# Kernel optimization log

Hardware: AMD Instinct MI355X
Metric: run time of the kernel (lower is better)

The kernel has to match this reference:

```python
import jax, jax.numpy as jnp
import numpy as np

B, N, D, H, E = 128, 256, 256, 8, 524288
RATIO = 0.5
HD = D // H
K_SEL = int(N * RATIO)  # nodes kept per graph


def setup_inputs() -> dict:
    key = jax.random.key(0)
    ks = jax.random.split(key, 12)
    embeddings = jax.random.normal(ks[0], (B, N, D), dtype=jnp.float32)
    mask = jnp.ones((B, N), dtype=bool)
    dist = jax.random.uniform(ks[1], (B, N, N), dtype=jnp.float32)
    # within-graph random edges, offset per graph
    epg = E // B
    src = jax.random.randint(ks[2], (B, epg), 0, N)
    dst = jax.random.randint(ks[3], (B, epg), 0, N)
    off = (jnp.arange(B) * N)[:, None]
    edge_index = jnp.stack([(src + off).reshape(-1), (dst + off).reshape(-1)]).astype(jnp.int64)
    batch = jnp.repeat(jnp.arange(B, dtype=jnp.int64), N)
    s = 1.0 / np.sqrt(D)
    Wq = jax.random.normal(ks[4], (D, D), jnp.float32) * s
    Wk = jax.random.normal(ks[5], (D, D), jnp.float32) * s
    Wv = jax.random.normal(ks[6], (D, D), jnp.float32) * s
    Wo = jax.random.normal(ks[7], (D, D), jnp.float32) * s
    bq = jnp.zeros((D,), jnp.float32)
    bk = jnp.zeros((D,), jnp.float32)
    bv = jnp.zeros((D,), jnp.float32)
    bo = jnp.zeros((D,), jnp.float32)
    pool_w = jax.random.normal(ks[8], (D,), jnp.float32) * s
    return dict(embeddings=embeddings, mask=mask, dist=dist, edge_index=edge_index,
                batch=batch, Wq=Wq, bq=bq, Wk=Wk, bk=bk, Wv=Wv, bv=bv, Wo=Wo, bo=bo,
                pool_w=pool_w)


def _mha(x, mask, dist, Wq, bq, Wk, bk, Wv, bv, Wo, bo):
    # x: [B,N,D]; dist used as additive attention bias; mask: [B,N] key mask
    q = (x @ Wq + bq).reshape(B, N, H, HD).transpose(0, 2, 1, 3)  # bhnd
    k = (x @ Wk + bk).reshape(B, N, H, HD).transpose(0, 2, 1, 3)
    v = (x @ Wv + bv).reshape(B, N, H, HD).transpose(0, 2, 1, 3)
    scores = jnp.einsum('bhnd,bhmd->bhnm', q, k) / jnp.sqrt(jnp.float32(HD))
    scores = scores + dist[:, None]  # broadcast bias over heads
    scores = jnp.where(mask[:, None, None, :], scores, jnp.float32(-1e9))
    attn = jax.nn.softmax(scores, axis=-1)
    out = jnp.einsum('bhnm,bhmd->bhnd', attn, v)
    out = out.transpose(0, 2, 1, 3).reshape(B, N, D)
    return out @ Wo + bo


def reference(embeddings, mask, dist, edge_index, batch, Wq, bq, Wk, bk, Wv, bv, Wo, bo, pool_w):
    encoder_result = _mha(embeddings, mask, dist, Wq, bq, Wk, bk, Wv, bv, Wo, bo)
    # encoder_result[mask] -> sparse node features; mask is all-true so shape is [B*N, D]
    x = encoder_result.reshape(B * N, D)

    # ---- TopKPooling (PyG semantics): score = x.w/||w||, keep top ceil(ratio*N)/graph ----
    score = (x @ pool_w) / jnp.linalg.norm(pool_w)          # [B*N]
    vals, idx = jax.lax.top_k(score.reshape(B, N), K_SEL)    # per-graph top-k
    perm = (idx + (jnp.arange(B) * N)[:, None]).reshape(-1)  # [B*K] global node ids
    sub_x = x[perm] * jnp.tanh(vals).reshape(-1, 1)
    sub_batch = batch[perm]

    # relabel nodes: new id = position in perm (PyG ordering); dropped -> sentinel
    n_keep = B * K_SEL
    sentinel = n_keep
    new_id = jnp.full((B * N,), sentinel, dtype=edge_index.dtype).at[perm].set(
        jnp.arange(n_keep, dtype=edge_index.dtype))
    row = new_id[edge_index[0]]
    col = new_id[edge_index[1]]
    valid = (row < sentinel) & (col < sentinel)
    row = jnp.where(valid, row, sentinel)
    col = jnp.where(valid, col, sentinel)
    # sort_edge_index: row-major sort; invalid (sentinel) edges pushed to the end
    order = jnp.argsort(row * (sentinel + 1) + col)
    sub_edge_index = jnp.stack([row, col])[:, order]
    return encoder_result, sub_x, sub_edge_index, sub_batch
```

## Files before the change

kernel.cpp:

```cpp
#include <hip/hip_runtime.h>
#include <math.h>

#define Bg   128
#define Ng   256
#define Dg   256
#define Hg   8
#define HDg  32
#define Eg   524288
#define Kg   128
#define BNg  32768
#define SENT 16384

using bf16x8 = __attribute__((ext_vector_type(8))) short;
using f32x4  = __attribute__((ext_vector_type(4))) float;

__device__ inline void split2(float x, short &h, short &l) {
    unsigned u = __float_as_uint(x);
    h = (short)(u >> 16);
    float hf = __uint_as_float(u & 0xffff0000u);
    float r = x - hf;
    l = (short)(__float_as_uint(r) >> 16);
}
__device__ inline unsigned pack2(short a, short b) {
    return (unsigned)(unsigned short)a | ((unsigned)(unsigned short)b << 16);
}
__device__ inline void gload16(const void* g, void* l) {
    __builtin_amdgcn_global_load_lds(
        (const __attribute__((address_space(1))) unsigned*)g,
        (__attribute__((address_space(3))) unsigned*)l, 16, 0, 0);
}

__global__ __launch_bounds__(256) void split_x(
    const float* __restrict__ x, short* __restrict__ xh, short* __restrict__ xl)
{
    size_t i = ((size_t)blockIdx.x * 256 + threadIdx.x) * 8;
    float4 a = *(const float4*)(x + i);
    float4 b = *(const float4*)(x + i + 4);
    float v[8] = {a.x,a.y,a.z,a.w,b.x,b.y,b.z,b.w};
    short h[8], l[8];
    #pragma unroll
    for (int j = 0; j < 8; ++j) split2(v[j], h[j], l[j]);
    uint4 uh, ul;
    uh.x = pack2(h[0],h[1]); uh.y = pack2(h[2],h[3]);
    uh.z = pack2(h[4],h[5]); uh.w = pack2(h[6],h[7]);
    ul.x = pack2(l[0],l[1]); ul.y = pack2(l[2],l[3]);
    ul.z = pack2(l[4],l[5]); ul.w = pack2(l[6],l[7]);
    *(uint4*)(xh + i) = uh;
    *(uint4*)(xl + i) = ul;
}

__global__ __launch_bounds__(256) void wprep(
    const float* __restrict__ Wq, const float* __restrict__ Wk,
    const float* __restrict__ Wv, const float* __restrict__ Wo,
    short* __restrict__ WTh, short* __restrict__ WTl)
{
    __shared__ float t[64][65];
    const int bid = blockIdx.x;
    const int mat = bid >> 4;
    const int kt = (bid >> 2) & 3, nt = bid & 3;
    const float* W = (mat==0) ? Wq : (mat==1) ? Wk : (mat==2) ? Wv : Wo;
    const int tid = threadIdx.x;
    const int r = tid >> 2, c4 = tid & 3;
    #pragma unroll
    for (int i = 0; i < 4; ++i) {
        float4 v = *(const float4*)(W + (size_t)(kt*64 + r)*256 + nt*64 + c4*16 + i*4);
        t[r][c4*16 + i*4 + 0] = v.x; t[r][c4*16 + i*4 + 1] = v.y;
        t[r][c4*16 + i*4 + 2] = v.z; t[r][c4*16 + i*4 + 3] = v.w;
    }
    __syncthreads();
    const int n = r, k0 = c4 * 16;
    short hb[16], lb[16];
    #pragma unroll
    for (int i = 0; i < 16; ++i) split2(t[k0 + i][n], hb[i], lb[i]);
    size_t base = (size_t)mat*65536 + (size_t)(nt*64 + n)*256 + kt*64 + k0;
    uint4 uh0, uh1, ul0, ul1;
    uh0.x=pack2(hb[0],hb[1]);  uh0.y=pack2(hb[2],hb[3]);  uh0.z=pack2(hb[4],hb[5]);  uh0.w=pack2(hb[6],hb[7]);
    uh1.x=pack2(hb[8],hb[9]);  uh1.y=pack2(hb[10],hb[11]);uh1.z=pack2(hb[12],hb[13]);uh1.w=pack2(hb[14],hb[15]);
    ul0.x=pack2(lb[0],lb[1]);  ul0.y=pack2(lb[2],lb[3]);  ul0.z=pack2(lb[4],lb[5]);  ul0.w=pack2(lb[6],lb[7]);
    ul1.x=pack2(lb[8],lb[9]);  ul1.y=pack2(lb[10],lb[11]);ul1.z=pack2(lb[12],lb[13]);ul1.w=pack2(lb[14],lb[15]);
    *(uint4*)&WTh[base]     = uh0; *(uint4*)&WTh[base + 8] = uh1;
    *(uint4*)&WTl[base]     = ul0; *(uint4*)&WTl[base + 8] = ul1;
}

__global__ __launch_bounds__(512, 4) void qkv_mm(
    const short* __restrict__ xh, const short* __restrict__ xl,
    const short* __restrict__ WTh, const short* __restrict__ WTl,
    const float* __restrict__ bq, const float* __restrict__ bk, const float* __restrict__ bv,
    short* __restrict__ Qh, short* __restrict__ Ql,
    short* __restrict__ Kh, short* __restrict__ Kl,
    short* __restrict__ Vh, short* __restrict__ Vl)
{
    const int z = blockIdx.z;
    const float* bias = (z==0) ? bq : (z==1) ? bk : bv;
    short* outH       = (z==0) ? Qh : (z==1) ? Kh : Vh;
    short* outL       = (z==0) ? Ql : (z==1) ? Kl : Vl;
    const float scale = (z==0) ? 0.17677669529663687f : 1.0f;
    const short* bth = WTh + (size_t)z * 65536;
    const short* btl = WTl + (size_t)z * 65536;
    __shared__ __align__(16) short lds[2][16384];
    const int tid = threadIdx.x;
    const int lane = tid & 63, w = tid >> 6;
    const int g = lane >> 4, li = lane & 15;
    const int wr = w >> 2, wc = w & 3;
    const int m0 = blockIdx.x * 128, n0 = blockIdx.y * 128;
    const int sr = tid >> 2, sc = (tid & 3) * 8;
    const int wbase = w * 512;
    f32x4 acc[4][2];
    #pragma unroll
    for (int i = 0; i < 4; ++i)
        #pragma unroll
        for (int j = 0; j < 2; ++j) acc[i][j] = (f32x4){0.f,0.f,0.f,0.f};

    {
        size_t ga = (size_t)(m0 + sr)*256 + sc;
        size_t gb = (size_t)(n0 + sr)*256 + sc;
        gload16(xh + ga,  &lds[0][        wbase]);
        gload16(xl + ga,  &lds[0][ 4096 + wbase]);
        gload16(bth + gb, &lds[0][ 8192 + wbase]);
        gload16(btl + gb, &lds[0][12288 + wbase]);
    }
    __syncthreads();

    for (int k = 0; k < 8; ++k) {
        const int cur = k & 1;
        if (k < 7) {
            const int nb = cur ^ 1;
            int k0n = (k+1)*32;
            size_t ga = (size_t)(m0 + sr)*256 + k0n + sc;
            size_t gb = (size_t)(n0 + sr)*256 + k0n + sc;
            gload16(xh + ga,  &lds[nb][        wbase]);
            gload16(xl + ga,  &lds[nb][ 4096 + wbase]);
            gload16(bth + gb, &lds[nb][ 8192 + wbase]);
            gload16(btl + gb, &lds[nb][12288 + wbase]);
        }
        bf16x8 ah[4], al[4], bh[2], bl[2];
        #pragma unroll
        for (int i = 0; i < 4; ++i) {
            int row = wr*64 + i*16 + li;
            ah[i] = *(const bf16x8*)&lds[cur][       row*32 + g*8];
            al[i] = *(const bf16x8*)&lds[cur][4096 + row*32 + g*8];
        }
        #pragma unroll
        for (int j = 0; j < 2; ++j) {
            int row = wc*32 + j*16 + li;
            bh[j] = *(const bf16x8*)&lds[cur][ 8192 + row*32 + g*8];
            bl[j] = *(const bf16x8*)&lds[cur][12288 + row*32 + g*8];
        }
        #pragma unroll
        for (int i = 0; i < 4; ++i)
            #pragma unroll
            for (int j = 0; j < 2; ++j) {
                acc[i][j] = __builtin_amdgcn_mfma_f32_16x16x32_bf16(bh[j], ah[i], acc[i][j], 0,0,0);
                acc[i][j] = __builtin_amdgcn_mfma_f32_16x16x32_bf16(bl[j], ah[i], acc[i][j], 0,0,0);
                acc[i][j] = __builtin_amdgcn_mfma_f32_16x16x32_bf16(bh[j], al[i], acc[i][j], 0,0,0);
            }
        __syncthreads();
    }
    #pragma unroll
    for (int i = 0; i < 4; ++i) {
        int mrow = m0 + wr*64 + i*16 + li;
        int b = mrow >> 8, nn = mrow & 255;
        #pragma unroll
        for (int j = 0; j < 2; ++j) {
            int c0 = n0 + wc*32 + j*16 + g*4;
            int h = c0 >> 5, hd = c0 & 31;
            float4 bi = *(const float4*)(bias + c0);
            float v0 = (acc[i][j][0] + bi.x) * scale;
            float v1 = (acc[i][j][1] + bi.y) * scale;
            float v2 = (acc[i][j][2] + bi.z) * scale;
            float v3 = (acc[i][j][3] + bi.w) * scale;
            short h0,l0,h1,l1,h2,l2,h3,l3;
            split2(v0,h0,l0); split2(v1,h1,l1); split2(v2,h2,l2); split2(v3,h3,l3);
            uint2 hiq, loq;
            hiq.x = pack2(h0,h1); hiq.y = pack2(h2,h3);
            loq.x = pack2(l0,l1); loq.y = pack2(l2,l3);
            size_t idx = ((size_t)(b*Hg + h)*Ng + nn)*HDg + hd;
            *(uint2*)&outH[idx] = hiq;
            *(uint2*)&outL[idx] = loq;
        }
    }
}

__global__ __launch_bounds__(512, 4) void attn_mfma(
    const short* __restrict__ Qh, const short* __restrict__ Ql,
    const short* __restrict__ Kh, const short* __restrict__ Kl,
    const short* __restrict__ Vh, const short* __restrict__ Vl,
    const float* __restrict__ dist,
    short* __restrict__ AOh, short* __restrict__ AOl)
{
    __shared__ __align__(16) short Khi [2][32][40];
    __shared__ __align__(16) short Klo [2][32][40];
    __shared__ __align__(16) short Vthi[2][32][40];
    __shared__ __align__(16) short Vtlo[2][32][40];
    __shared__ __align__(16) short Phi [8][32][40];
    __shared__ __align__(16) short Plo [8][32][40];

    const int i0 = blockIdx.x;
    const int xcd = i0 & 7;
    const int m_  = i0 >> 3;
    const int h   = m_ & 7;
    const int b   = (m_ >> 3) * 8 + xcd;
    const int bh  = b * 8 + h;

    const int tid = threadIdx.x;
    const int w = tid >> 6;
    const int lane = tid & 63;
    const int g = lane >> 4;
    const int li = lane & 15;
    const int q0 = w * 32;
    const int skey = tid >> 4;
    const int se0  = (tid & 15) * 2;
    const float* dall = dist + (size_t)b*Ng*Ng;

    bf16x8 qh[2], ql[2];
    #pragma unroll
    for (int tq = 0; tq < 2; ++tq) {
        size_t qoff = ((size_t)bh * Ng + q0 + tq*16 + li) * HDg + g*8;
        qh[tq] = *(const bf16x8*)(Qh + qoff);
        ql[tq] = *(const bf16x8*)(Ql + qoff);
    }

    {
        size_t koff = ((size_t)bh*Ng + skey) * HDg + se0;
        unsigned kh1 = *(const unsigned*)(Kh + koff);
        unsigned kl1 = *(const unsigned*)(Kl + koff);
        unsigned vh1 = *(const unsigned*)(Vh + koff);
        unsigned vl1 = *(const unsigned*)(Vl + koff);
        *(unsigned*)&Khi[0][skey][se0] = kh1;
        *(unsigned*)&Klo[0][skey][se0] = kl1;
        Vthi[0][se0+0][skey] = (short)(vh1 & 0xffff);
        Vthi[0][se0+1][skey] = (short)(vh1 >> 16);
        Vtlo[0][se0+0][skey] = (short)(vl1 & 0xffff);
        Vtlo[0][se0+1][skey] = (short)(vl1 >> 16);
    }
    __syncthreads();

    f32x4 O[2][2];
    #pragma unroll
    for (int tq=0;tq<2;++tq)
        #pragma unroll
        for (int td=0;td<2;++td) O[tq][td] = (f32x4){0.f,0.f,0.f,0.f};
    float lpart[2] = {0.f, 0.f};

    for (int ch = 0; ch < 8; ++ch) {
        const int cur = ch & 1;
        const bool pref = (ch < 7);
        unsigned khr, klr, vhr, vlr;
        if (pref) {
            size_t koff = ((size_t)bh*Ng + (ch+1)*32 + skey) * HDg + se0;
            khr = *(const unsigned*)(Kh + koff);
            klr = *(const unsigned*)(Kl + koff);
            vhr = *(const unsigned*)(Vh + koff);
            vlr = *(const unsigned*)(Vl + koff);
        }
        f32x4 sacc[2][2];
        #pragma unroll
        for (int tq = 0; tq < 2; ++tq)
            #pragma unroll
            for (int tc = 0; tc < 2; ++tc) {
                const float* dp = dall + (size_t)(q0 + tq*16 + li)*Ng + ch*32 + tc*16 + g*4;
                float4 dv = *(const float4*)dp;
                sacc[tq][tc] = (f32x4){dv.x, dv.y, dv.z, dv.w};
            }
        bf16x8 kbh[2], kbl[2];
        #pragma unroll
        for (int tc = 0; tc < 2; ++tc) {
            kbh[tc] = *(const bf16x8*)&Khi[cur][tc*16+li][g*8];
            kbl[tc] = *(const bf16x8*)&Klo[cur][tc*16+li][g*8];
        }
        #pragma unroll
        for (int tq = 0; tq < 2; ++tq)
            #pragma unroll
            for (int tc = 0; tc < 2; ++tc) {
                sacc[tq][tc] = __builtin_amdgcn_mfma_f32_16x16x32_bf16(kbh[tc], qh[tq], sacc[tq][tc], 0,0,0);
                sacc[tq][tc] = __builtin_amdgcn_mfma_f32_16x16x32_bf16(kbl[tc], qh[tq], sacc[tq][tc], 0,0,0);
                sacc[tq][tc] = __builtin_amdgcn_mfma_f32_16x16x32_bf16(kbh[tc], ql[tq], sacc[tq][tc], 0,0,0);
            }
        #pragma unroll
        for (int tq = 0; tq < 2; ++tq)
            #pragma unroll
            for (int tc = 0; tc < 2; ++tc) {
                float p0 = __expf(sacc[tq][tc][0] - 16.f);
                float p1 = __expf(sacc[tq][tc][1] - 16.f);
                float p2 = __expf(sacc[tq][tc][2] - 16.f);
                float p3 = __expf(sacc[tq][tc][3] - 16.f);
                lpart[tq] += p0; lpart[tq] += p1; lpart[tq] += p2; lpart[tq] += p3;
                unsigned u0 = __float_as_uint(p0), u1 = __float_as_uint(p1);
                unsigned u2 = __float_as_uint(p2), u3 = __float_as_uint(p3);
                float r0 = p0 - __uint_as_float(u0 & 0xffff0000u);
                float r1 = p1 - __uint_as_float(u1 & 0xffff0000u);
                float r2 = p2 - __uint_as_float(u2 & 0xffff0000u);
                float r3 = p3 - __uint_as_float(u3 & 0xffff0000u);
                uint2 hiq, loq;
                hiq.x = (u0 >> 16) | (u1 & 0xffff0000u);
                hiq.y = (u2 >> 16) | (u3 & 0xffff0000u);
                loq.x = (__float_as_uint(r0) >> 16) | (__float_as_uint(r1) & 0xffff0000u);
                loq.y = (__float_as_uint(r2) >> 16) | (__float_as_uint(r3) & 0xffff0000u);
                *(uint2*)&Phi[w][tq*16 + li][tc*16 + g*4] = hiq;
                *(uint2*)&Plo[w][tq*16 + li][tc*16 + g*4] = loq;
            }
        bf16x8 vbh[2], vbl[2];
        #pragma unroll
        for (int td = 0; td < 2; ++td) {
            vbh[td] = *(const bf16x8*)&Vthi[cur][td*16+li][g*8];
            vbl[td] = *(const bf16x8*)&Vtlo[cur][td*16+li][g*8];
        }
        #pragma unroll
        for (int tq = 0; tq < 2; ++tq) {
            bf16x8 ph = *(const bf16x8*)&Phi[w][tq*16+li][g*8];
            bf16x8 pl = *(const bf16x8*)&Plo[w][tq*16+li][g*8];
            #pragma unroll
            for (int td = 0; td < 2; ++td) {
                O[tq][td] = __builtin_amdgcn_mfma_f32_16x16x32_bf16(vbh[td], ph, O[tq][td], 0,0,0);
                O[tq][td] = __builtin_amdgcn_mfma_f32_16x16x32_bf16(vbl[td], ph, O[tq][td], 0,0,0);
                O[tq][td] = __builtin_amdgcn_mfma_f32_16x16x32_bf16(vbh[td], pl, O[tq][td], 0,0,0);
            }
        }
        if (pref) {
            const int nb = cur ^ 1;
            *(unsigned*)&Khi[nb][skey][se0] = khr;
            *(unsigned*)&Klo[nb][skey][se0] = klr;
            Vthi[nb][se0+0][skey] = (short)(vhr & 0xffff);
            Vthi[nb][se0+1][skey] = (short)(vhr >> 16);
            Vtlo[nb][se0+0][skey] = (short)(vlr & 0xffff);
            Vtlo[nb][se0+1][skey] = (short)(vlr >> 16);
        }
        __syncthreads();
    }
    float inv[2];
    #pragma unroll
    for (int tq = 0; tq < 2; ++tq) {
        float s = lpart[tq];
        s += __shfl_xor(s, 16);
        s += __shfl_xor(s, 32);
        inv[tq] = 1.f / s;
    }
    #pragma unroll
    for (int tq = 0; tq < 2; ++tq)
        #pragma unroll
        for (int td = 0; td < 2; ++td) {
            float v0 = O[tq][td][0] * inv[tq];
            float v1 = O[tq][td][1] * inv[tq];
            float v2 = O[tq][td][2] * inv[tq];
            float v3 = O[tq][td][3] * inv[tq];
            unsigned u0 = __float_as_uint(v0), u1 = __float_as_uint(v1);
            unsigned u2 = __float_as_uint(v2), u3 = __float_as_uint(v3);
            float r0 = v0 - __uint_as_float(u0 & 0xffff0000u);
            float r1 = v1 - __uint_as_float(u1 & 0xffff0000u);
            float r2 = v2 - __uint_as_float(u2 & 0xffff0000u);
            float r3 = v3 - __uint_as_float(u3 & 0xffff0000u);
            uint2 hiq, loq;
            hiq.x = (u0 >> 16) | (u1 & 0xffff0000u);
            hiq.y = (u2 >> 16) | (u3 & 0xffff0000u);
            loq.x = (__float_as_uint(r0) >> 16) | (__float_as_uint(r1) & 0xffff0000u);
            loq.y = (__float_as_uint(r2) >> 16) | (__float_as_uint(r3) & 0xffff0000u);
            int q = q0 + tq*16 + li;
            size_t base = ((size_t)b*Ng + q)*Dg + h*HDg + td*16 + g*4;
            *(uint2*)&AOh[base] = hiq;
            *(uint2*)&AOl[base] = loq;
        }
}

__global__ __launch_bounds__(512, 4) void out_mm(
    const short* __restrict__ aoh, const short* __restrict__ aol,
    const short* __restrict__ bth, const short* __restrict__ btl,
    const float* __restrict__ bo, float* __restrict__ enc)
{
    __shared__ __align__(16) short lds[2][16384];
    const int tid = threadIdx.x;
    const int lane = tid & 63, w = tid >> 6;
    const int g = lane >> 4, li = lane & 15;
    const int wr = w >> 2, wc = w & 3;
    const int m0 = blockIdx.x * 128, n0 = blockIdx.y * 128;
    const int sr = tid >> 2, sc = (tid & 3) * 8;
    const int wbase = w * 512;
    f32x4 acc[4][2];
    #pragma unroll
    for (int i = 0; i < 4; ++i)
        #pragma unroll
        for (int j = 0; j < 2; ++j) acc[i][j] = (f32x4){0.f,0.f,0.f,0.f};

    {
        size_t ga = (size_t)(m0 + sr)*256 + sc;
        size_t gb = (size_t)(n0 + sr)*256 + sc;
        gload16(aoh + ga, &lds[0][        wbase]);
        gload16(aol + ga, &lds[0][ 4096 + wbase]);
        gload16(bth + gb, &lds[0][ 8192 + wbase]);
        gload16(btl + gb, &lds[0][12288 + wbase]);
    }
    __syncthreads();

    for (int k = 0; k < 8; ++k) {
        const int cur = k & 1;
        if (k < 7) {
            const int nb = cur ^ 1;
            int k0n = (k+1)*32;
            size_t ga = (size_t)(m0 + sr)*256 + k0n + sc;
            size_t gb = (size_t)(n0 + sr)*256 + k0n + sc;
            gload16(aoh + ga, &lds[nb][        wbase]);
            gload16(aol + ga, &lds[nb][ 4096 + wbase]);
            gload16(bth + gb, &lds[nb][ 8192 + wbase]);
            gload16(btl + gb, &lds[nb][12288 + wbase]);
        }
        bf16x8 ah[4], al[4], bh[2], bl[2];
        #pragma unroll
        for (int i = 0; i < 4; ++i) {
            int row = wr*64 + i*16 + li;
            ah[i] = *(const bf16x8*)&lds[cur][       row*32 + g*8];
            al[i] = *(const bf16x8*)&lds[cur][4096 + row*32 + g*8];
        }
        #pragma unroll
        for (int j = 0; j < 2; ++j) {
            int row = wc*32 + j*16 + li;
            bh[j] = *(const bf16x8*)&lds[cur][ 8192 + row*32 + g*8];
            bl[j] = *(const bf16x8*)&lds[cur][12288 + row*32 + g*8];
        }
        #pragma unroll
        for (int i = 0; i < 4; ++i)
            #pragma unroll
            for (int j = 0; j < 2; ++j) {
                acc[i][j] = __builtin_amdgcn_mfma_f32_16x16x32_bf16(bh[j], ah[i], acc[i][j], 0,0,0);
                acc[i][j] = __builtin_amdgcn_mfma_f32_16x16x32_bf16(bl[j], ah[i], acc[i][j], 0,0,0);
                acc[i][j] = __builtin_amdgcn_mfma_f32_16x16x32_bf16(bh[j], al[i], acc[i][j], 0,0,0);
            }
        __syncthreads();
    }
    #pragma unroll
    for (int i = 0; i < 4; ++i) {
        int mrow = m0 + wr*64 + i*16 + li;
        #pragma unroll
        for (int j = 0; j < 2; ++j) {
            int c0 = n0 + wc*32 + j*16 + g*4;
            float4 bo4 = *(const float4*)(bo + c0);
            float4 v;
            v.x = acc[i][j][0] + bo4.x;
            v.y = acc[i][j][1] + bo4.y;
            v.z = acc[i][j][2] + bo4.z;
            v.w = acc[i][j][3] + bo4.w;
            *(float4*)&enc[(size_t)mrow*Dg + c0] = v;
        }
    }
}

__global__ __launch_bounds__(256) void score_kernel(
    const float* __restrict__ enc, const float* __restrict__ pw, float* __restrict__ score)
{
    int row  = blockIdx.x * 8 + (threadIdx.x >> 5);
    int lane = threadIdx.x & 31;
    const float* r = enc + (size_t)row * Dg;
    float s = 0.f;
    for (int d = lane; d < Dg; d += 32) s = fmaf(r[d], pw[d], s);
    #pragma unroll
    for (int off = 16; off > 0; off >>= 1) s += __shfl_xor(s, off);
    if (lane == 0) score[row] = s;
}

__global__ void norm_kernel(const float* __restrict__ pw, float* __restrict__ inv_norm)
{
    int t = threadIdx.x;
    float s = 0.f;
    for (int d = t; d < Dg; d += 64) s = fmaf(pw[d], pw[d], s);
    #pragma unroll
    for (int off = 32; off > 0; off >>= 1) s += __shfl_xor(s, off);
    if (t == 0) *inv_norm = 1.0f / sqrtf(s);
}

__global__ __launch_bounds__(256) void topk_kernel(
    const float* __restrict__ score, float* __restrict__ vals, int* __restrict__ idxs,
    int* __restrict__ new_id, float* __restrict__ out_batch)
{
    __shared__ float sh[Ng];
    int bgr = blockIdx.x, t = threadIdx.x;
    float mine = score[(size_t)bgr * Ng + t];
    sh[t] = mine;
    __syncthreads();
    int cnt = 0;
    for (int j = 0; j < Ng; ++j) {
        float v = sh[j];
        cnt += (v > mine || (v == mine && j < t)) ? 1 : 0;
    }
    if (cnt < Kg) {
        int pos = bgr * Kg + cnt;
        vals[pos] = mine;
        idxs[pos] = t;
        new_id[bgr * Ng + t] = pos;
        out_batch[pos] = (float)bgr;
    } else {
        new_id[bgr * Ng + t] = SENT;
    }
}

__global__ __launch_bounds__(256) void subx_kernel(
    const float* __restrict__ enc, const float* __restrict__ vals,
    const int* __restrict__ idxs, const float* __restrict__ inv_norm,
    float* __restrict__ out_subx)
{
    int j    = blockIdx.x * 4 + (threadIdx.x >> 6);
    int lane = threadIdx.x & 63;
    int bgr  = j >> 7;
    int src  = bgr * Ng + idxs[j];
    float scale = tanhf(vals[j] * (*inv_norm));
    float4 v = reinterpret_cast<const float4*>(enc + (size_t)src * Dg)[lane];
    v.x *= scale; v.y *= scale; v.z *= scale; v.w *= scale;
    reinterpret_cast<float4*>(out_subx + (size_t)j * Dg)[lane] = v;
}

__global__ __launch_bounds__(256) void edge_hist(
    const int* __restrict__ ei, const int* __restrict__ new_id, int* __restrict__ counts)
{
    int e = blockIdx.x * 256 + threadIdx.x;
    int r = new_id[ei[e]];
    int c = new_id[ei[Eg + e]];
    if (r != SENT && c != SENT) atomicAdd(&counts[r], 1);
}

__global__ __launch_bounds__(256) void scan_kernel(
    const int* __restrict__ counts, int* __restrict__ offsets)
{
    __shared__ int sums[256];
    int t = threadIdx.x;
    int base = t * 64;
    int s = 0;
    for (int i = 0; i < 64; ++i) s += counts[base + i];
    sums[t] = s;
    __syncthreads();
    for (int off = 1; off < 256; off <<= 1) {
        int add = (t >= off) ? sums[t - off] : 0;
        __syncthreads();
        sums[t] += add;
        __syncthreads();
    }
    int run = sums[t] - s;
    for (int i = 0; i < 64; ++i) { offsets[base + i] = run; run += counts[base + i]; }
    if (t == 255) offsets[SENT] = run;
}

__global__ __launch_bounds__(256) void edge_scatter(
    const int* __restrict__ ei, const int* __restrict__ new_id,
    const int* __restrict__ offsets, int* __restrict__ cursor, int* __restrict__ bucket)
{
    int e = blockIdx.x * 256 + threadIdx.x;
    int r = new_id[ei[e]];
    int c = new_id[ei[Eg + e]];
    if (r != SENT && c != SENT) {
        int pos = offsets[r] + atomicAdd(&cursor[r], 1);
        bucket[pos] = c;
    }
}

__global__ __launch_bounds__(256) void edge_sort_emit(
    const int* __restrict__ offsets, int* bucket, float* __restrict__ out_edges)
{
    int r = blockIdx.x * 256 + threadIdx.x;
    int s = offsets[r], e = offsets[r + 1];
    for (int i = s + 1; i < e; ++i) {
        int key = bucket[i];
        int j = i - 1;
        while (j >= s && bucket[j] > key) { bucket[j+1] = bucket[j]; --j; }
        bucket[j+1] = key;
    }
    float rf = (float)r;
    for (int i = s; i < e; ++i) {
        out_edges[i]      = rf;
        out_edges[Eg + i] = (float)bucket[i];
    }
}

__global__ __launch_bounds__(256) void edge_fill(
    const int* __restrict__ offsets, float* __restrict__ out_edges)
{
    int p = blockIdx.x * 256 + threadIdx.x;
    if (p >= offsets[SENT]) {
        out_edges[p]      = (float)SENT;
        out_edges[Eg + p] = (float)SENT;
    }
}

extern "C" void kernel_launch(void* const* d_in, const int* in_sizes, int n_in,
                              void* d_out, int out_size, void* d_ws, size_t ws_size,
                              hipStream_t stream)
{
    const float* x    = (const float*)d_in[0];
    const float* dist = (const float*)d_in[2];
    const int*   ei   = (const int*)d_in[3];
    const float* Wq = (const float*)d_in[5];
    const float* bq = (const float*)d_in[6];
    const float* Wk = (const float*)d_in[7];
    const float* bk = (const float*)d_in[8];
    const float* Wv = (const float*)d_in[9];
    const float* bv = (const float*)d_in[10];
    const float* Wo = (const float*)d_in[11];
    const float* bo = (const float*)d_in[12];
    const float* pw = (const float*)d_in[13];

    float* out       = (float*)d_out;
    float* enc_out   = out;
    float* subx_out  = out + 8388608;
    float* edge_out  = out + 12582912;
    float* batch_out = out + 13631488;

    float* ws      = (float*)d_ws;
    short* Qh      = (short*)ws;
    short* Ql      = (short*)(ws + 4194304);
    short* Kh      = (short*)(ws + 8388608);
    short* Kl      = (short*)(ws + 12582912);
    short* Vh      = (short*)(ws + 16777216);
    short* Vl      = (short*)(ws + 20971520);
    short* xh      = (short*)(ws + 25165824);
    short* xl      = (short*)(ws + 29360128);
    short* AOh     = xh;
    short* AOl     = xl;
    short* WTh     = (short*)(ws + 33554432);
    short* WTl     = (short*)(ws + 33685504);
    float* score   = ws + 33816576;
    float* vals    = ws + 33849344;
    int*   idxs    = (int*)(ws + 33865728);
    int*   new_id  = (int*)(ws + 33882112);
    int*   counts  = (int*)(ws + 33914880);
    int*   offsets = (int*)(ws + 33931264);
    int*   cursor  = (int*)(ws + 33947680);
    float* inv_nm  = ws + 33964064;
    int*   bucket  = (int*)(ws + 33964096);

    hipMemsetAsync(counts, 0, SENT * sizeof(int), stream);
    hipMemsetAsync(cursor, 0, SENT * sizeof(int), stream);

    split_x       <<<dim3(4096),               256, 0, stream>>>(x, xh, xl);
    wprep         <<<dim3(64),                 256, 0, stream>>>(Wq, Wk, Wv, Wo, WTh, WTl);
    norm_kernel   <<<dim3(1),                   64, 0, stream>>>(pw, inv_nm);
    qkv_mm        <<<dim3(BNg/128, Dg/128, 3), 512, 0, stream>>>(xh, xl, WTh, WTl, bq, bk, bv,
                                                                 Qh, Ql, Kh, Kl, Vh, Vl);
    attn_mfma     <<<dim3(Bg*Hg),              512, 0, stream>>>(Qh, Ql, Kh, Kl, Vh, Vl, dist, AOh, AOl);
    out_mm        <<<dim3(BNg/128, Dg/128),    512, 0, stream>>>(AOh, AOl, WTh + 3*65536, WTl + 3*65536, bo, enc_out);
    score_kernel  <<<dim3(BNg/8),              256, 0, stream>>>(enc_out, pw, score);
    topk_kernel   <<<dim3(Bg),                 256, 0, stream>>>(score, vals, idxs, new_id, batch_out);
    subx_kernel   <<<dim3((Bg*Kg)/4),          256, 0, stream>>>(enc_out, vals, idxs, inv_nm, subx_out);
    edge_hist     <<<dim3(Eg/256),             256, 0, stream>>>(ei, new_id, counts);
    scan_kernel   <<<dim3(1),                  256, 0, stream>>>(counts, offsets);
    edge_scatter  <<<dim3(Eg/256),             256, 0, stream>>>(ei, new_id, offsets, cursor, bucket);
    edge_sort_emit<<<dim3(SENT/256),           256, 0, stream>>>(offsets, bucket, edge_out);
    edge_fill     <<<dim3(Eg/256),             256, 0, stream>>>(offsets, edge_out);
    (void)in_sizes; (void)n_in; (void)out_size; (void)ws_size;
}
```

Before: 227.9 us.

## Prefetch dist bias one chunk ahead and fuse pooling score into out_mm

The attention kernel now loads the dist bias tiles for the next key chunk during the current chunk, using two register sets alternated in an unrolled loop, so global load latency overlaps with MFMA work. The separate score_kernel is removed. out_mm now computes per-row partial dot products with pool_w in its epilogue and writes 8 partial sums per row, which topk_kernel adds up. This drops one kernel launch and a full re-read of the encoder output, at the cost of more registers in attention and a different floating-point summation order for scores, which could change top-k tie-breaking.

```diff
diff --git a/kernel.cpp b/kernel.cpp
--- a/kernel.cpp
+++ b/kernel.cpp
@@ -220,6 +220,15 @@
         ql[tq] = *(const bf16x8*)(Ql + qoff);
     }
 
+    f32x4 dA[2][2], dB[2][2];
+    #pragma unroll
+    for (int tq = 0; tq < 2; ++tq)
+        #pragma unroll
+        for (int tc = 0; tc < 2; ++tc) {
+            const float* dp = dall + (size_t)(q0 + tq*16 + li)*Ng + tc*16 + g*4;
+            float4 dv = *(const float4*)dp;
+            dA[tq][tc] = (f32x4){dv.x, dv.y, dv.z, dv.w};
+        }
     {
         size_t koff = ((size_t)bh*Ng + skey) * HDg + se0;
         unsigned kh1 = *(const unsigned*)(Kh + koff);
@@ -242,11 +251,20 @@
         for (int td=0;td<2;++td) O[tq][td] = (f32x4){0.f,0.f,0.f,0.f};
     float lpart[2] = {0.f, 0.f};
 
-    for (int ch = 0; ch < 8; ++ch) {
+    auto body = [&](int ch, f32x4 (&dcur)[2][2], f32x4 (&dnx)[2][2]) {
         const int cur = ch & 1;
         const bool pref = (ch < 7);
         unsigned khr, klr, vhr, vlr;
         if (pref) {
+            const float* dbase = dall + (ch+1)*32;
+            #pragma unroll
+            for (int tq = 0; tq < 2; ++tq)
+                #pragma unroll
+                for (int tc = 0; tc < 2; ++tc) {
+                    const float* dp = dbase + (size_t)(q0 + tq*16 + li)*Ng + tc*16 + g*4;
+                    float4 dv = *(const float4*)dp;
+                    dnx[tq][tc] = (f32x4){dv.x, dv.y, dv.z, dv.w};
+                }
             size_t koff = ((size_t)bh*Ng + (ch+1)*32 + skey) * HDg + se0;
             khr = *(const unsigned*)(Kh + koff);
             klr = *(const unsigned*)(Kl + koff);
@@ -254,24 +272,17 @@
             vlr = *(const unsigned*)(Vl + koff);
         }
         f32x4 sacc[2][2];
+        bf16x8 kbh[2], kbl[2];
+        #pragma unroll
+        for (int tc = 0; tc < 2; ++tc) {
+            kbh[tc] = *(const bf16x8*)&Khi[cur][tc*16+li][g*8];
+            kbl[tc] = *(const bf16x8*)&Klo[cur][tc*16+li][g*8];
+        }
         #pragma unroll
         for (int tq = 0; tq < 2; ++tq)
             #pragma unroll
             for (int tc = 0; tc < 2; ++tc) {
-                const float* dp = dall + (size_t)(q0 + tq*16 + li)*Ng + ch*32 + tc*16 + g*4;
-                float4 dv = *(const float4*)dp;
-                sacc[tq][tc] = (f32x4){dv.x, dv.y, dv.z, dv.w};
-            }
-        bf16x8 kbh[2], kbl[2];
-        #pragma unroll
-        for (int tc = 0; tc < 2; ++tc) {
-            kbh[tc] = *(const bf16x8*)&Khi[cur][tc*16+li][g*8];
-            kbl[tc] = *(const bf16x8*)&Klo[cur][tc*16+li][g*8];
-        }
-        #pragma unroll
-        for (int tq = 0; tq < 2; ++tq)
-            #pragma unroll
-            for (int tc = 0; tc < 2; ++tc) {
+                sacc[tq][tc] = dcur[tq][tc];
                 sacc[tq][tc] = __builtin_amdgcn_mfma_f32_16x16x32_bf16(kbh[tc], qh[tq], sacc[tq][tc], 0,0,0);
                 sacc[tq][tc] = __builtin_amdgcn_mfma_f32_16x16x32_bf16(kbl[tc], qh[tq], sacc[tq][tc], 0,0,0);
                 sacc[tq][tc] = __builtin_amdgcn_mfma_f32_16x16x32_bf16(kbh[tc], ql[tq], sacc[tq][tc], 0,0,0);
@@ -326,7 +337,14 @@
             Vtlo[nb][se0+1][skey] = (short)(vlr >> 16);
         }
         __syncthreads();
-    }
+    };
+
+    #pragma unroll
+    for (int ch8 = 0; ch8 < 8; ch8 += 2) {
+        body(ch8,     dA, dB);
+        body(ch8 + 1, dB, dA);
+    }
+
     float inv[2];
     #pragma unroll
     for (int tq = 0; tq < 2; ++tq) {
@@ -364,7 +382,8 @@
 __global__ __launch_bounds__(512, 4) void out_mm(
     const short* __restrict__ aoh, const short* __restrict__ aol,
     const short* __restrict__ bth, const short* __restrict__ btl,
-    const float* __restrict__ bo, float* __restrict__ enc)
+    const float* __restrict__ bo, const float* __restrict__ pw,
+    float* __restrict__ enc, float* __restrict__ score_part)
 {
     __shared__ __align__(16) short lds[2][16384];
     const int tid = threadIdx.x;
@@ -425,34 +444,28 @@
             }
         __syncthreads();
     }
+    const int pslot = blockIdx.y * 4 + wc;
     #pragma unroll
     for (int i = 0; i < 4; ++i) {
         int mrow = m0 + wr*64 + i*16 + li;
+        float s = 0.f;
         #pragma unroll
         for (int j = 0; j < 2; ++j) {
             int c0 = n0 + wc*32 + j*16 + g*4;
             float4 bo4 = *(const float4*)(bo + c0);
+            float4 pw4 = *(const float4*)(pw + c0);
             float4 v;
             v.x = acc[i][j][0] + bo4.x;
             v.y = acc[i][j][1] + bo4.y;
             v.z = acc[i][j][2] + bo4.z;
             v.w = acc[i][j][3] + bo4.w;
             *(float4*)&enc[(size_t)mrow*Dg + c0] = v;
-        }
-    }
-}
-
-__global__ __launch_bounds__(256) void score_kernel(
-    const float* __restrict__ enc, const float* __restrict__ pw, float* __restrict__ score)
-{
-    int row  = blockIdx.x * 8 + (threadIdx.x >> 5);
-    int lane = threadIdx.x & 31;
-    const float* r = enc + (size_t)row * Dg;
-    float s = 0.f;
-    for (int d = lane; d < Dg; d += 32) s = fmaf(r[d], pw[d], s);
-    #pragma unroll
-    for (int off = 16; off > 0; off >>= 1) s += __shfl_xor(s, off);
-    if (lane == 0) score[row] = s;
+            s += v.x*pw4.x + v.y*pw4.y + v.z*pw4.z + v.w*pw4.w;
+        }
+        s += __shfl_xor(s, 16);
+        s += __shfl_xor(s, 32);
+        if (g == 0) score_part[(size_t)pslot * BNg + mrow] = s;
+    }
 }
 
 __global__ void norm_kernel(const float* __restrict__ pw, float* __restrict__ inv_norm)
@@ -466,12 +479,15 @@
 }
 
 __global__ __launch_bounds__(256) void topk_kernel(
-    const float* __restrict__ score, float* __restrict__ vals, int* __restrict__ idxs,
+    const float* __restrict__ score_part, float* __restrict__ vals, int* __restrict__ idxs,
     int* __restrict__ new_id, float* __restrict__ out_batch)
 {
     __shared__ float sh[Ng];
     int bgr = blockIdx.x, t = threadIdx.x;
-    float mine = score[(size_t)bgr * Ng + t];
+    int row = bgr * Ng + t;
+    float mine = 0.f;
+    #pragma unroll
+    for (int p = 0; p < 8; ++p) mine += score_part[(size_t)p * BNg + row];
     sh[t] = mine;
     __syncthreads();
     int cnt = 0;
@@ -612,7 +628,6 @@
     short* AOl     = xl;
     short* WTh     = (short*)(ws + 33554432);
     short* WTl     = (short*)(ws + 33685504);
-    float* score   = ws + 33816576;
     float* vals    = ws + 33849344;
     int*   idxs    = (int*)(ws + 33865728);
     int*   new_id  = (int*)(ws + 33882112);
@@ -621,6 +636,7 @@
     int*   cursor  = (int*)(ws + 33947680);
     float* inv_nm  = ws + 33964064;
     int*   bucket  = (int*)(ws + 33964096);
+    float* score_part = ws + 34488384;
 
     hipMemsetAsync(counts, 0, SENT * sizeof(int), stream);
     hipMemsetAsync(cursor, 0, SENT * sizeof(int), stream);
@@ -631,9 +647,9 @@
     qkv_mm        <<<dim3(BNg/128, Dg/128, 3), 512, 0, stream>>>(xh, xl, WTh, WTl, bq, bk, bv,
                                                                  Qh, Ql, Kh, Kl, Vh, Vl);
     attn_mfma     <<<dim3(Bg*Hg),              512, 0, stream>>>(Qh, Ql, Kh, Kl, Vh, Vl, dist, AOh, AOl);
-    out_mm        <<<dim3(BNg/128, Dg/128),    512, 0, stream>>>(AOh, AOl, WTh + 3*65536, WTl + 3*65536, bo, enc_out);
-    score_kernel  <<<dim3(BNg/8),              256, 0, stream>>>(enc_out, pw, score);
-    topk_kernel   <<<dim3(Bg),                 256, 0, stream>>>(score, vals, idxs, new_id, batch_out);
+    out_mm        <<<dim3(BNg/128, Dg/128),    512, 0, stream>>>(AOh, AOl, WTh + 3*65536, WTl + 3*65536,
+                                                                 bo, pw, enc_out, score_part);
+    topk_kernel   <<<dim3(Bg),                 256, 0, stream>>>(score_part, vals, idxs, new_id, batch_out);
     subx_kernel   <<<dim3((Bg*Kg)/4),          256, 0, stream>>>(enc_out, vals, idxs, inv_nm, subx_out);
     edge_hist     <<<dim3(Eg/256),             256, 0, stream>>>(ei, new_id, counts);
     scan_kernel   <<<dim3(1),                  256, 0, stream>>>(counts, offsets);
```

Result: slower. 276.8 us (+21.5%).
